# Performance work log

Hardware: AMD Instinct MI355X
Metric: run time of the kernel (lower is better)

## Reference

```python
import jax, jax.numpy as jnp
import numpy as np

B, IN, H, K = 4096, 1024, 1024, 32  # batch, input_size, hidden_size, inner_hidden


def setup_inputs() -> dict:
    key = jax.random.key(0)
    ks = jax.random.split(key, 11)
    stdv = 1.0 / np.sqrt(H)
    u = lambda k, shp: jax.random.uniform(k, shp, jnp.float32, -stdv, stdv)
    return {
        "x": jax.random.normal(ks[0], (B, IN), jnp.float32),
        "h_prev": jax.random.normal(ks[1], (B, H), jnp.float32),
        "c_prev": jax.random.normal(ks[2], (B, H), jnp.float32),
        "Wg": u(ks[3], (3 * H, IN + H)),
        "bg": u(ks[4], (3 * H,)),
        "Wc": u(ks[5], (2 * H, IN + H)),
        "bc": u(ks[6], (2 * H,)),
        "W1": u(ks[7], (K, 2)),
        "b1": u(ks[8], (K,)),
        "W2": u(ks[9], (1, K)),
        "b2": u(ks[10], (1,)),
    }


def reference(x, h_prev, c_prev, Wg, bg, Wc, bc, W1, b1, W2, b2):
    combined = jnp.concatenate([x, h_prev], axis=1)          # [B, IN+H]
    gates = combined @ Wg.T + bg                              # [B, 3H]
    i, f, o = jnp.split(jax.nn.sigmoid(gates), 3, axis=1)     # each [B, H]
    cell_raw = combined @ Wc.T + bc                           # [B, 2H]
    pairs = cell_raw.reshape(B, H, 2)                         # [B, H, 2]
    hid = jax.nn.relu(jnp.einsum('bhp,kp->bhk', pairs, W1) + b1)  # [B, H, K]
    g = jnp.einsum('bhk,ok->bho', hid, W2)[..., 0] + b2[0]    # [B, H]
    c_next = f * c_prev + i * g
    h_next = o * jnp.tanh(c_next)
    return (h_next, c_next)
```

## Files before the change

kernel.cpp:

```cpp
#include <hip/hip_runtime.h>
#include <hip/hip_bf16.h>

#define BB   4096
#define INW  1024
#define HH   1024
#define KIN  2048
#define NG   5120
#define KH   32
#define FPG  10
#define NTG  32

typedef __bf16 bf16;
typedef __bf16 bf16x4 __attribute__((ext_vector_type(4)));
typedef __bf16 bf16x8 __attribute__((ext_vector_type(8)));
typedef float  floatx4 __attribute__((ext_vector_type(4)));

#define GLD16(gp, lp)                                                          \
  __builtin_amdgcn_global_load_lds(                                            \
      (__attribute__((address_space(1))) const void*)(gp),                     \
      (__attribute__((address_space(3))) void*)(lp), 16, 0, 0)

#define NC4  (BB * KIN / 4)
#define NW8  (NG * KIN / 8)

__global__ __launch_bounds__(256) void prep(
    const float* __restrict__ x, const float* __restrict__ h,
    const float* __restrict__ Wg, const float* __restrict__ Wc,
    bf16* __restrict__ comb, bf16* __restrict__ Wb) {
  int i = blockIdx.x * 256 + threadIdx.x;
  if (i < NC4) {
    int e = i * 4;
    int b = e >> 11;
    int c = e & (KIN - 1);
    const float* src = (c < INW) ? (x + (size_t)b * INW + c)
                                 : (h + (size_t)b * HH + (c - INW));
    float4 v = *(const float4*)src;
    bf16x4 o4;
    o4[0] = (bf16)v.x; o4[1] = (bf16)v.y; o4[2] = (bf16)v.z; o4[3] = (bf16)v.w;
    *(bf16x4*)(comb + e) = o4;
  } else {
    int o = i - NC4;
    if (o < NW8) {
      int lane = o & 63;
      int t    = o >> 6;
      int f    = t % FPG;
      t        = t / FPG;
      int kk   = t & 63;
      int nt   = t >> 6;
      int q    = f / 5;
      int g    = f - q * 5;
      int hcol = nt * 32 + q * 16 + (lane & 15);
      int k    = kk * 32 + (lane >> 4) * 8;
      const float* src = (g < 3)
          ? (Wg + (size_t)(g * HH + hcol) * KIN + k)
          : (Wc + (size_t)(2 * hcol + (g - 3)) * KIN + k);
      float4 v0 = *(const float4*)src;
      float4 v1 = *(const float4*)(src + 4);
      bf16x8 ov;
      ov[0] = (bf16)v0.x; ov[1] = (bf16)v0.y; ov[2] = (bf16)v0.z; ov[3] = (bf16)v0.w;
      ov[4] = (bf16)v1.x; ov[5] = (bf16)v1.y; ov[6] = (bf16)v1.z; ov[7] = (bf16)v1.w;
      *(bf16x8*)(Wb + (size_t)o * 8) = ov;
    }
  }
}

__global__ __launch_bounds__(256, 2) void gemm_fused(
    const bf16* __restrict__ A, const bf16* __restrict__ Bm,
    const float* __restrict__ c_prev, const float* __restrict__ bg,
    const float* __restrict__ bc, const float* __restrict__ W1,
    const float* __restrict__ b1, const float* __restrict__ W2,
    const float* __restrict__ b2, float* __restrict__ h_next,
    float* __restrict__ c_next) {
  __shared__ bf16 As[128 * 128];

  const int tid  = threadIdx.x;
  const int wave = tid >> 6;
  const int lane = tid & 63;

  const int bid = blockIdx.y * gridDim.x + blockIdx.x;
  const int swz = (bid & 7) * 128 + (bid >> 3);
  const int m0  = (swz & 31) * 128;
  const int nt  = swz >> 5;

  const int wm = (wave >> 1) * 64;
  const int q  = wave & 1;
  const int lr = lane & 15;
  const int qd = lane >> 4;

  const bf16* Bq = Bm + ((size_t)(nt * 640 + q * 5) * 64 + lane) * 8;

  floatx4 acc[4][5] = {};

  for (int kt = 0; kt < KIN / 128; ++kt) {
    bf16x8 bfr[4][5];
#pragma unroll
    for (int ks = 0; ks < 4; ++ks)
#pragma unroll
      for (int ni = 0; ni < 5; ++ni)
        bfr[ks][ni] =
            *(const bf16x8*)(Bq + ((size_t)((kt * 4 + ks) * FPG + ni) << 9));

    __syncthreads();
#pragma unroll
    for (int j = 0; j < 8; ++j) {
      int s   = j * 256 + tid;
      int row = s >> 4;
      int c   = (s & 15) ^ (row & 15);
      GLD16(A + (size_t)(m0 + row) * KIN + kt * 128 + c * 8,
            As + (size_t)(j * 256 + wave * 64) * 8);
    }
    __syncthreads();

#pragma unroll
    for (int ks = 0; ks < 4; ++ks) {
      bf16x8 af[4];
#pragma unroll
      for (int mi = 0; mi < 4; ++mi) {
        int row  = wm + mi * 16 + lr;
        int slot = (ks * 4 + qd) ^ lr;
        af[mi] = *(const bf16x8*)&As[(row << 7) + (slot << 3)];
      }
#pragma unroll
      for (int mi = 0; mi < 4; ++mi)
#pragma unroll
        for (int ni = 0; ni < 5; ++ni)
          acc[mi][ni] = __builtin_amdgcn_mfma_f32_16x16x32_bf16(
              af[mi], bfr[ks][ni], acc[mi][ni], 0, 0, 0);
    }
  }

  const int h   = nt * 32 + q * 16 + lr;
  const float bgi = bg[h];
  const float bgf = bg[HH + h];
  const float bgo = bg[2 * HH + h];
  const float bc0 = bc[2 * h];
  const float bc1 = bc[2 * h + 1];
  const float gb  = b2[0];

  float p0[16], p1[16], ga[16];
#pragma unroll
  for (int mi = 0; mi < 4; ++mi)
#pragma unroll
    for (int r = 0; r < 4; ++r) {
      p0[mi * 4 + r] = acc[mi][3][r] + bc0;
      p1[mi * 4 + r] = acc[mi][4][r] + bc1;
      ga[mi * 4 + r] = gb;
    }
#pragma unroll
  for (int k = 0; k < KH; ++k) {
    float w0 = W1[2 * k], w1 = W1[2 * k + 1], bk = b1[k], wk = W2[k];
#pragma unroll
    for (int e = 0; e < 16; ++e) {
      float hv = fmaf(p0[e], w0, fmaf(p1[e], w1, bk));
      hv = fmaxf(hv, 0.0f);
      ga[e] = fmaf(hv, wk, ga[e]);
    }
  }

#pragma unroll
  for (int mi = 0; mi < 4; ++mi)
#pragma unroll
    for (int r = 0; r < 4; ++r) {
      int b    = m0 + wm + mi * 16 + qd * 4 + r;
      size_t o = (size_t)b * HH + h;
      float si = 1.0f / (1.0f + __expf(-(acc[mi][0][r] + bgi)));
      float sf = 1.0f / (1.0f + __expf(-(acc[mi][1][r] + bgf)));
      float so = 1.0f / (1.0f + __expf(-(acc[mi][2][r] + bgo)));
      float cn = fmaf(sf, c_prev[o], si * ga[mi * 4 + r]);
      float e2 = __expf(2.0f * cn);
      float th = 1.0f - 2.0f / (e2 + 1.0f);
      h_next[o] = so * th;
      c_next[o] = cn;
    }
}

extern "C" void kernel_launch(void* const* d_in, const int* in_sizes, int n_in,
                              void* d_out, int out_size, void* d_ws, size_t ws_size,
                              hipStream_t stream) {
  const float* x      = (const float*)d_in[0];
  const float* h_prev = (const float*)d_in[1];
  const float* c_prev = (const float*)d_in[2];
  const float* Wg     = (const float*)d_in[3];
  const float* bg     = (const float*)d_in[4];
  const float* Wc     = (const float*)d_in[5];
  const float* bc     = (const float*)d_in[6];
  const float* W1     = (const float*)d_in[7];
  const float* b1     = (const float*)d_in[8];
  const float* W2     = (const float*)d_in[9];
  const float* b2     = (const float*)d_in[10];
  float* out = (float*)d_out;

  char* ws = (char*)d_ws;
  bf16* comb = (bf16*)ws;
  bf16* Wb   = (bf16*)(ws + (size_t)BB * KIN * 2);

  prep<<<(NC4 + NW8 + 255) / 256, 256, 0, stream>>>(x, h_prev, Wg, Wc, comb, Wb);

  dim3 grid(BB / 128, NTG);
  gemm_fused<<<grid, 256, 0, stream>>>(comb, Wb, c_prev, bg, bc, W1, b1, W2,
                                       b2, out, out + (size_t)BB * HH);
}
```

Measured before the change: 236.6 us.

## Double-buffer B fragments, relayout weight prep, raise GEMM occupancy

The GEMM used to preload all 20 B fragments per k-tile into registers. It now keeps two 5-fragment buffers that are refilled between MFMA steps, which frees registers so launch bounds can allow 3 blocks per CU. The prep kernel's weight conversion is changed so that each block reads full contiguous source rows (coalesced reads), and the B layout is reindexed to match. The activation conversion now handles 8 elements per thread. The risk is that the smaller prefetch depth exposes more global-load latency for B inside the k-loop.

```diff
diff --git a/kernel.cpp b/kernel.cpp
--- a/kernel.cpp
+++ b/kernel.cpp
@@ -20,51 +20,77 @@
       (__attribute__((address_space(1))) const void*)(gp),                     \
       (__attribute__((address_space(3))) void*)(lp), 16, 0, 0)
 
-#define NC4  (BB * KIN / 4)
-#define NW8  (NG * KIN / 8)
+#define NCB  4096
+#define NWB  1280
 
 __global__ __launch_bounds__(256) void prep(
     const float* __restrict__ x, const float* __restrict__ h,
     const float* __restrict__ Wg, const float* __restrict__ Wc,
     bf16* __restrict__ comb, bf16* __restrict__ Wb) {
-  int i = blockIdx.x * 256 + threadIdx.x;
-  if (i < NC4) {
-    int e = i * 4;
+  int tid = threadIdx.x;
+  if (blockIdx.x < NCB) {
+    int e = (blockIdx.x * 256 + tid) * 8;
     int b = e >> 11;
     int c = e & (KIN - 1);
     const float* src = (c < INW) ? (x + (size_t)b * INW + c)
                                  : (h + (size_t)b * HH + (c - INW));
-    float4 v = *(const float4*)src;
-    bf16x4 o4;
-    o4[0] = (bf16)v.x; o4[1] = (bf16)v.y; o4[2] = (bf16)v.z; o4[3] = (bf16)v.w;
-    *(bf16x4*)(comb + e) = o4;
+    float4 v0 = *(const float4*)src;
+    float4 v1 = *(const float4*)(src + 4);
+    bf16x8 ov;
+    ov[0] = (bf16)v0.x; ov[1] = (bf16)v0.y; ov[2] = (bf16)v0.z; ov[3] = (bf16)v0.w;
+    ov[4] = (bf16)v1.x; ov[5] = (bf16)v1.y; ov[6] = (bf16)v1.z; ov[7] = (bf16)v1.w;
+    *(bf16x8*)(comb + e) = ov;
   } else {
-    int o = i - NC4;
-    if (o < NW8) {
-      int lane = o & 63;
-      int t    = o >> 6;
-      int f    = t % FPG;
-      t        = t / FPG;
-      int kk   = t & 63;
-      int nt   = t >> 6;
-      int q    = f / 5;
-      int g    = f - q * 5;
-      int hcol = nt * 32 + q * 16 + (lane & 15);
-      int k    = kk * 32 + (lane >> 4) * 8;
+    int w   = blockIdx.x - NCB;
+    int nt  = w / 40;
+    int rem = w - nt * 40;
+    int f   = rem >> 2;
+    int rp  = rem & 3;
+    int q   = f / 5;
+    int g   = f - q * 5;
+    int kk  = tid >> 2;
+    int kq  = tid & 3;
+    size_t wbase = ((size_t)(nt * FPG + f) * 64 + kk) * 64 + kq * 16;
+#pragma unroll
+    for (int r4 = 0; r4 < 4; ++r4) {
+      int s    = rp * 4 + r4;
+      int hcol = nt * 32 + q * 16 + s;
       const float* src = (g < 3)
-          ? (Wg + (size_t)(g * HH + hcol) * KIN + k)
-          : (Wc + (size_t)(2 * hcol + (g - 3)) * KIN + k);
+          ? (Wg + (size_t)(g * HH + hcol) * KIN + tid * 8)
+          : (Wc + (size_t)(2 * hcol + (g - 3)) * KIN + tid * 8);
       float4 v0 = *(const float4*)src;
       float4 v1 = *(const float4*)(src + 4);
       bf16x8 ov;
       ov[0] = (bf16)v0.x; ov[1] = (bf16)v0.y; ov[2] = (bf16)v0.z; ov[3] = (bf16)v0.w;
       ov[4] = (bf16)v1.x; ov[5] = (bf16)v1.y; ov[6] = (bf16)v1.z; ov[7] = (bf16)v1.w;
-      *(bf16x8*)(Wb + (size_t)o * 8) = ov;
+      *(bf16x8*)(Wb + (wbase + s) * 8) = ov;
     }
   }
 }
 
-__global__ __launch_bounds__(256, 2) void gemm_fused(
+#define LOADB(buf, ksl)                                                        \
+  _Pragma("unroll")                                                            \
+  for (int ni = 0; ni < 5; ++ni)                                               \
+    buf[ni] = *(const bf16x8*)(Bq + (size_t)ni * 32768 + (size_t)(ksl) * 512);
+
+#define MFMAS(buf, ks)                                                         \
+  {                                                                            \
+    bf16x8 af[4];                                                              \
+    _Pragma("unroll")                                                          \
+    for (int mi = 0; mi < 4; ++mi) {                                           \
+      int row  = wm + mi * 16 + lr;                                            \
+      int slot = ((ks) * 4 + qd) ^ lr;                                         \
+      af[mi] = *(const bf16x8*)&As[(row << 7) + (slot << 3)];                  \
+    }                                                                          \
+    _Pragma("unroll")                                                          \
+    for (int mi = 0; mi < 4; ++mi)                                             \
+      _Pragma("unroll")                                                        \
+      for (int ni = 0; ni < 5; ++ni)                                           \
+        acc[mi][ni] = __builtin_amdgcn_mfma_f32_16x16x32_bf16(                 \
+            af[mi], buf[ni], acc[mi][ni], 0, 0, 0);                            \
+  }
+
+__global__ __launch_bounds__(256, 3) void gemm_fused(
     const bf16* __restrict__ A, const bf16* __restrict__ Bm,
     const float* __restrict__ c_prev, const float* __restrict__ bg,
     const float* __restrict__ bc, const float* __restrict__ W1,
@@ -87,18 +113,14 @@
   const int lr = lane & 15;
   const int qd = lane >> 4;
 
-  const bf16* Bq = Bm + ((size_t)(nt * 640 + q * 5) * 64 + lane) * 8;
+  const bf16* Bq = Bm + ((size_t)(nt * FPG + q * 5) * 4096 + lane) * 8;
 
   floatx4 acc[4][5] = {};
 
   for (int kt = 0; kt < KIN / 128; ++kt) {
-    bf16x8 bfr[4][5];
-#pragma unroll
-    for (int ks = 0; ks < 4; ++ks)
-#pragma unroll
-      for (int ni = 0; ni < 5; ++ni)
-        bfr[ks][ni] =
-            *(const bf16x8*)(Bq + ((size_t)((kt * 4 + ks) * FPG + ni) << 9));
+    bf16x8 bf0[5], bf1[5];
+    LOADB(bf0, kt * 4 + 0);
+    LOADB(bf1, kt * 4 + 1);
 
     __syncthreads();
 #pragma unroll
@@ -111,22 +133,12 @@
     }
     __syncthreads();
 
-#pragma unroll
-    for (int ks = 0; ks < 4; ++ks) {
-      bf16x8 af[4];
-#pragma unroll
-      for (int mi = 0; mi < 4; ++mi) {
-        int row  = wm + mi * 16 + lr;
-        int slot = (ks * 4 + qd) ^ lr;
-        af[mi] = *(const bf16x8*)&As[(row << 7) + (slot << 3)];
-      }
-#pragma unroll
-      for (int mi = 0; mi < 4; ++mi)
-#pragma unroll
-        for (int ni = 0; ni < 5; ++ni)
-          acc[mi][ni] = __builtin_amdgcn_mfma_f32_16x16x32_bf16(
-              af[mi], bfr[ks][ni], acc[mi][ni], 0, 0, 0);
-    }
+    MFMAS(bf0, 0);
+    LOADB(bf0, kt * 4 + 2);
+    MFMAS(bf1, 1);
+    LOADB(bf1, kt * 4 + 3);
+    MFMAS(bf0, 2);
+    MFMAS(bf1, 3);
   }
 
   const int h   = nt * 32 + q * 16 + lr;
@@ -194,7 +206,7 @@
   bf16* comb = (bf16*)ws;
   bf16* Wb   = (bf16*)(ws + (size_t)BB * KIN * 2);
 
-  prep<<<(NC4 + NW8 + 255) / 256, 256, 0, stream>>>(x, h_prev, Wg, Wc, comb, Wb);
+  prep<<<NCB + NWB, 256, 0, stream>>>(x, h_prev, Wg, Wc, comb, Wb);
 
   dim3 grid(BB / 128, NTG);
   gemm_fused<<<grid, 256, 0, stream>>>(comb, Wb, c_prev, bg, bc, W1, b1, W2,
```

New measurement: 358.7 us. +51.6%, slower.
